# Optimization experiments

Measured on AMD Instinct MI355X. Metric: run time of the kernel, lower is better.

## Reference

```python
import jax, jax.numpy as jnp
import numpy as np

# DeepSeek-style MLA sparse decode: absorbed W_UK/W_UV matmuls in latent space,
# top-k sparse gather from the (kv_lora_rank + rope) latent KV cache.

B, H, S, K = 32, 16, 8192, 2048
L, DN, DR, DV, DM = 512, 128, 64, 128, 2048
SCALE = 1.0 / np.sqrt(DN + DR)  # softmax scale over full qk_head_dim = 192


def setup_inputs() -> dict:
    key = jax.random.key(0)
    ks = jax.random.split(key, 8)
    return {
        "q_nope": jax.random.normal(ks[0], (B, H, DN), dtype=jnp.float32),
        "q_pe": jax.random.normal(ks[1], (B, H, DR), dtype=jnp.float32),  # post-RoPE
        "kv_c": jax.random.normal(ks[2], (B, S, L), dtype=jnp.float32),   # latent cache
        "k_pe": jax.random.normal(ks[3], (B, S, DR), dtype=jnp.float32),  # post-RoPE cache
        "W_UK": jax.random.normal(ks[4], (L, H, DN), dtype=jnp.float32) * 0.02,
        "W_UV": jax.random.normal(ks[5], (L, H, DV), dtype=jnp.float32) * 0.02,
        "W_O": jax.random.normal(ks[6], (H * DV, DM), dtype=jnp.float32) * 0.02,
        "topk_indices": jax.random.randint(ks[7], (B, K), 0, S, dtype=jnp.int32),
    }


def reference(q_nope, q_pe, kv_c, k_pe, W_UK, W_UV, W_O, topk_indices):
    b, h, _ = q_nope.shape
    seq = kv_c.shape[1]
    # absorb q_nope into latent space: [B,H,L]
    q_latent = jnp.einsum('bhd,lhd->bhl', q_nope, W_UK)
    # top-k sparse gather from paged latent cache (-1 == invalid slot)
    valid = topk_indices >= 0                         # [B,K]
    idx = jnp.clip(topk_indices, 0, seq - 1)
    kv_sel = jnp.take_along_axis(kv_c, idx[:, :, None], axis=1)   # [B,K,L]
    kpe_sel = jnp.take_along_axis(k_pe, idx[:, :, None], axis=1)  # [B,K,DR]
    # attention scores: latent part + rope part, fused scale
    scores = (jnp.einsum('bhl,bkl->bhk', q_latent, kv_sel)
              + jnp.einsum('bhr,bkr->bhk', q_pe, kpe_sel)) * SCALE
    scores = jnp.where(valid[:, None, :], scores, -jnp.inf)
    attn = jax.nn.softmax(scores, axis=-1)            # [B,H,K]
    # weighted sum in latent space, then up-project with W_UV
    o_latent = jnp.einsum('bhk,bkl->bhl', attn, kv_sel)
    o = jnp.einsum('bhl,lhv->bhv', o_latent, W_UV)    # [B,H,DV]
    return o.reshape(b, h * o.shape[-1]) @ W_O        # [B,DM]
```

## Files before the change

### kernel.cpp

```cpp
#include <hip/hip_runtime.h>
#include <hip/hip_bf16.h>
#include <cstdint>
#include <cstddef>

constexpr int NB = 32;
constexpr int NH = 16;
constexpr int NS = 8192;
constexpr int NK = 2048;
constexpr int NL = 512;
constexpr int NDR = 64;
constexpr int NDV = 128;
constexpr int NDM = 2048;
constexpr int NDN = 128;
constexpr float SCALE = 0.07216878364870322f;

constexpr int NSPLIT = 32;
constexpr int KC = NK / NSPLIT;
constexpr int ND = NL + NDR;
constexpr int NSUB_D = ND / 16;
constexpr int NS2 = 64;

typedef __attribute__((ext_vector_type(8))) short sh8;
typedef __attribute__((ext_vector_type(4))) float f32x4;

__device__ __forceinline__ short bf16c(float f) {
  union { float f; uint32_t u; } v; v.f = f;
  uint32_t r = v.u + 0x7fffu + ((v.u >> 16) & 1u);
  return (short)(r >> 16);
}

__device__ __forceinline__ float bf2f(short s) {
  union { uint32_t u; float f; } v; v.u = ((uint32_t)(uint16_t)s) << 16;
  return v.f;
}

__device__ __forceinline__ sh8 pack_bf8(float4 a, float4 b) {
  sh8 f;
  f[0] = bf16c(a.x); f[1] = bf16c(a.y); f[2] = bf16c(a.z); f[3] = bf16c(a.w);
  f[4] = bf16c(b.x); f[5] = bf16c(b.y); f[6] = bf16c(b.z); f[7] = bf16c(b.w);
  return f;
}

__global__ __launch_bounds__(256)
void k_qprep(const float* __restrict__ qn,
             const float* __restrict__ qpe,
             const float* __restrict__ wuk,
             short* __restrict__ qle) {
  const int h  = blockIdx.x & 15;
  const int lc = blockIdx.x >> 4;
  const int l0 = lc * 32;
  const int t  = threadIdx.x;
  __shared__ float wlds[32 * 136];
  __shared__ float qlds[32 * 136];

  #pragma unroll
  for (int j = 0; j < 4; ++j) {
    int idx = t + j * 256;
    int li  = idx >> 5;
    int d4  = (idx & 31) * 4;
    *(float4*)&wlds[li * 136 + d4] =
        *(const float4*)&wuk[((size_t)(l0 + li) * NH + h) * NDN + d4];
    *(float4*)&qlds[li * 136 + d4] =
        *(const float4*)&qn[((size_t)li * NH + h) * NDN + d4];
  }
  __syncthreads();

  const int b = t >> 3;
  #pragma unroll
  for (int j = 0; j < 4; ++j) {
    int li = (t & 7) + j * 8;
    float acc = 0.f;
    #pragma unroll
    for (int d4 = 0; d4 < NDN; d4 += 4) {
      float4 wv = *(float4*)&wlds[li * 136 + d4];
      float4 qv = *(float4*)&qlds[b * 136 + d4];
      acc += wv.x * qv.x + wv.y * qv.y + wv.z * qv.z + wv.w * qv.w;
    }
    qle[((size_t)b * NH + h) * ND + l0 + li] = bf16c(acc);
  }
  if (lc == 0) {
    #pragma unroll
    for (int j = 0; j < 8; ++j) {
      int i = t + j * 256;
      int bb = i >> 6, dr = i & 63;
      qle[((size_t)bb * NH + h) * ND + NL + dr] =
          bf16c(qpe[((size_t)bb * NH + h) * NDR + dr]);
    }
  }
}

__global__ __launch_bounds__(256, 2)
void k_attn(const float* __restrict__ kvc,
            const float* __restrict__ kpe,
            const int*   __restrict__ topk,
            const short* __restrict__ qle,
            float* __restrict__ pm,
            float* __restrict__ psum,
            unsigned short* __restrict__ po) {
  const int sp = blockIdx.x;
  const int b  = blockIdx.y;
  const int t  = threadIdx.x;
  const int w  = t >> 6;
  const int lane = t & 63;
  const int lg = lane >> 4;
  const int ln = lane & 15;

  __shared__ __align__(16) short kvs[(KC / 4) * NSUB_D * 64];
  __shared__ __align__(16) short plds[NH * 72];
  __shared__ float mlds[4 * NH];
  __shared__ float slds[4 * NH];

  {
    const int r = t >> 2, c8 = t & 3;
    int idx = topk[(size_t)b * NK + sp * KC + r];
    int id = idx < 0 ? 0 : (idx >= NS ? NS - 1 : idx);
    const float* rowc = kvc + ((size_t)b * NS + id) * NL;
    const float* rowp = kpe + ((size_t)b * NS + id) * NDR;
    #pragma unroll
    for (int g = 0; g < 3; ++g) {
      float4 va[6], vb[6];
      #pragma unroll
      for (int i = 0; i < 6; ++i) {
        int d0 = c8 * 8 + (g * 6 + i) * 32;
        const float* src = (d0 < NL) ? (rowc + d0) : (rowp + (d0 - NL));
        va[i] = *(const float4*)src;
        vb[i] = *(const float4*)(src + 4);
      }
      #pragma unroll
      for (int i = 0; i < 6; ++i) {
        int d0 = c8 * 8 + (g * 6 + i) * 32;
        int s = (r >> 2) * NSUB_D + (d0 >> 4);
        *(sh8*)&kvs[s * 64 + (r & 3) * 16 + (d0 & 15)] = pack_bf8(va[i], vb[i]);
      }
    }
  }
  __syncthreads();

  f32x4 accs = {0.f, 0.f, 0.f, 0.f};
  {
    const short* qrow = qle + ((size_t)b * NH + ln) * ND;
    int k = w * 16 + ln;
    int kbase = (k >> 2) * NSUB_D * 64 + (k & 3) * 16;
    #pragma unroll
    for (int kk = 0; kk < 18; ++kk) {
      int d0 = kk * 32 + lg * 8;
      sh8 qv = *(const sh8*)&qrow[d0];
      sh8 bfr = *(const sh8*)&kvs[kbase + (d0 >> 4) * 64 + (d0 & 15)];
      accs = __builtin_amdgcn_mfma_f32_16x16x32_bf16(qv, bfr, accs, 0, 0, 0);
    }
  }

  const int kq = w * 16 + ln;
  bool valid = topk[(size_t)b * NK + sp * KC + kq] >= 0;
  float sv[4], mx[4];
  #pragma unroll
  for (int q = 0; q < 4; ++q) {
    sv[q] = valid ? accs[q] * SCALE : -INFINITY;
    mx[q] = sv[q];
  }
  #pragma unroll
  for (int off = 1; off < 16; off <<= 1)
    #pragma unroll
    for (int q = 0; q < 4; ++q) mx[q] = fmaxf(mx[q], __shfl_xor(mx[q], off));
  if (ln == 0) {
    #pragma unroll
    for (int q = 0; q < 4; ++q) mlds[w * NH + lg * 4 + q] = mx[q];
  }
  __syncthreads();

  float pr[4], sm[4];
  #pragma unroll
  for (int q = 0; q < 4; ++q) {
    int h = lg * 4 + q;
    float m = fmaxf(fmaxf(mlds[h], mlds[NH + h]),
                    fmaxf(mlds[2 * NH + h], mlds[3 * NH + h]));
    m = fmaxf(m, -1e30f);
    pr[q] = __expf(sv[q] - m);
    sm[q] = pr[q];
  }
  #pragma unroll
  for (int off = 1; off < 16; off <<= 1)
    #pragma unroll
    for (int q = 0; q < 4; ++q) sm[q] += __shfl_xor(sm[q], off);
  if (ln == 0) {
    #pragma unroll
    for (int q = 0; q < 4; ++q) slds[w * NH + lg * 4 + q] = sm[q];
  }
  #pragma unroll
  for (int q = 0; q < 4; ++q)
    plds[(lg * 4 + q) * 72 + kq] = bf16c(pr[q]);
  __syncthreads();

  if (t < NH) {
    float m = fmaxf(fmaxf(mlds[t], mlds[NH + t]),
                    fmaxf(mlds[2 * NH + t], mlds[3 * NH + t]));
    m = fmaxf(m, -1e30f);
    float s = slds[t] + slds[NH + t] + slds[2 * NH + t] + slds[3 * NH + t];
    pm[((size_t)b * NSPLIT + sp) * NH + t] = m;
    psum[((size_t)b * NSPLIT + sp) * NH + t] = s;
  }

  f32x4 acco[8];
  #pragma unroll
  for (int nt = 0; nt < 8; ++nt) acco[nt] = {0.f, 0.f, 0.f, 0.f};

  #pragma unroll
  for (int ks = 0; ks < 2; ++ks) {
    sh8 pa = *(const sh8*)&plds[ln * 72 + ks * 32 + lg * 8];
    int kb = ks * 32 + lg * 8;
    #pragma unroll
    for (int nt = 0; nt < 8; ++nt) {
      int l0 = w * 128 + nt * 16;
      int s = (kb >> 2) * NSUB_D + (l0 >> 4);
      const short* base = &kvs[s * 64 + ln];
      sh8 bv;
      #pragma unroll
      for (int j = 0; j < 4; ++j) bv[j] = base[j * 16];
      #pragma unroll
      for (int j = 0; j < 4; ++j) bv[4 + j] = base[NSUB_D * 64 + j * 16];
      acco[nt] = __builtin_amdgcn_mfma_f32_16x16x32_bf16(pa, bv, acco[nt], 0, 0, 0);
    }
  }

  unsigned short* dst = po + (((size_t)b * NSPLIT + sp) * NH) * NL;
  #pragma unroll
  for (int nt = 0; nt < 8; ++nt) {
    int l = w * 128 + nt * 16 + ln;
    #pragma unroll
    for (int q = 0; q < 4; ++q)
      dst[(size_t)(lg * 4 + q) * NL + l] = (unsigned short)bf16c(acco[nt][q]);
  }
}

__global__ __launch_bounds__(256)
void k_coef(const float* __restrict__ pm,
            const float* __restrict__ psum,
            float* __restrict__ coef) {
  int b = blockIdx.x;
  __shared__ float mm[NSPLIT * NH];
  __shared__ float ssum[NSPLIT * NH];
  int t = threadIdx.x;
  for (int i = t; i < NSPLIT * NH; i += 256) {
    mm[i] = pm[(size_t)b * NSPLIT * NH + i];
    ssum[i] = psum[(size_t)b * NSPLIT * NH + i];
  }
  __syncthreads();
  if (t < NH) {
    float M = -1e30f;
    #pragma unroll
    for (int sp = 0; sp < NSPLIT; ++sp) M = fmaxf(M, mm[sp * NH + t]);
    float S = 0.f;
    #pragma unroll
    for (int sp = 0; sp < NSPLIT; ++sp) S += ssum[sp * NH + t] * __expf(mm[sp * NH + t] - M);
    S = fmaxf(S, 1e-30f);
    #pragma unroll
    for (int sp = 0; sp < NSPLIT; ++sp)
      coef[((size_t)b * NSPLIT + sp) * NH + t] = __expf(mm[sp * NH + t] - M) / S;
  }
}

__global__ __launch_bounds__(256)
void k_combine(const float* __restrict__ coef,
               const unsigned short* __restrict__ po,
               const float* __restrict__ wuv,
               float* __restrict__ ov) {
  int bh = blockIdx.x;
  int b = bh >> 4, h = bh & 15;
  __shared__ float clds[NSPLIT];
  __shared__ float ol[NL];
  __shared__ float red[2][NDV];
  int t = threadIdx.x;
  if (t < NSPLIT) clds[t] = coef[((size_t)b * NSPLIT + t) * NH + h];
  __syncthreads();
  {
    float a0 = 0.f, a1 = 0.f;
    #pragma unroll
    for (int i = 0; i < NSPLIT; ++i) {
      uint32_t pv = *(const uint32_t*)&po[(((size_t)b * NSPLIT + i) * NH + h) * NL + 2 * t];
      a0 += clds[i] * bf2f((short)(pv & 0xffff));
      a1 += clds[i] * bf2f((short)(pv >> 16));
    }
    ol[2 * t] = a0;
    ol[2 * t + 1] = a1;
  }
  __syncthreads();
  {
    int v = t & (NDV - 1);
    int half = t >> 7;
    float a = 0.f;
    #pragma unroll 16
    for (int l = half * 256; l < half * 256 + 256; ++l)
      a += ol[l] * wuv[((size_t)l * NH + h) * NDV + v];
    red[half][v] = a;
  }
  __syncthreads();
  if (t < NDV) ov[(size_t)bh * NDV + t] = red[0][t] + red[1][t];
}

__global__ __launch_bounds__(256)
void k_gemm_part(const float* __restrict__ ov,
                 const float* __restrict__ wo,
                 float* __restrict__ gp) {
  int mc = blockIdx.x;
  int ns = blockIdx.y;
  __shared__ float oc[NB * 32];
  int t = threadIdx.x;
  for (int i = t; i < NB * 32; i += 256) {
    int b = i >> 5, n = i & 31;
    oc[i] = ov[(size_t)b * NDM + ns * 32 + n];
  }
  __syncthreads();
  float acc[NB];
  #pragma unroll
  for (int b = 0; b < NB; ++b) acc[b] = 0.f;
  int m = mc * 256 + t;
  #pragma unroll 8
  for (int n = 0; n < 32; ++n) {
    float wv = wo[(size_t)(ns * 32 + n) * NDM + m];
    #pragma unroll
    for (int b = 0; b < NB; ++b) acc[b] += oc[b * 32 + n] * wv;
  }
  #pragma unroll
  for (int b = 0; b < NB; ++b)
    gp[((size_t)ns * NB + b) * NDM + m] = acc[b];
}

__global__ __launch_bounds__(256)
void k_reduce(const float* __restrict__ gp, float* __restrict__ out) {
  int g = blockIdx.x * 256 + threadIdx.x;
  float a = 0.f;
  #pragma unroll 8
  for (int i = 0; i < NS2; ++i)
    a += gp[(size_t)i * (NB * NDM) + g];
  out[g] = a;
}

extern "C" void kernel_launch(void* const* d_in, const int* in_sizes, int n_in,
                              void* d_out, int out_size, void* d_ws, size_t ws_size,
                              hipStream_t stream) {
  const float* q_nope = (const float*)d_in[0];
  const float* q_pe   = (const float*)d_in[1];
  const float* kv_c   = (const float*)d_in[2];
  const float* k_pe   = (const float*)d_in[3];
  const float* W_UK   = (const float*)d_in[4];
  const float* W_UV   = (const float*)d_in[5];
  const float* W_O    = (const float*)d_in[6];
  const int*   topk   = (const int*)d_in[7];
  float* out = (float*)d_out;

  float* ws = (float*)d_ws;
  short* qle = (short*)ws;
  float* pm   = ws + 147456;
  float* psum = pm + 16384;
  unsigned short* po = (unsigned short*)(psum + 16384);
  float* coef = psum + 16384 + 4194304;
  float* ov   = coef + 16384;
  float* gp   = ov + 65536;

  k_qprep<<<256, 256, 0, stream>>>(q_nope, q_pe, W_UK, qle);
  k_attn<<<dim3(NSPLIT, NB), 256, 0, stream>>>(kv_c, k_pe, topk, qle,
                                               pm, psum, po);
  k_coef<<<NB, 256, 0, stream>>>(pm, psum, coef);
  k_combine<<<NB * NH, 256, 0, stream>>>(coef, po, W_UV, ov);
  k_gemm_part<<<dim3(8, NS2), 256, 0, stream>>>(ov, W_O, gp);
  k_reduce<<<(NB * NDM) / 256, 256, 0, stream>>>(gp, out);
}
```

Before: 90.57 us.

## Fold softmax coefficient kernel into combine and replace split-K reduce with atomics

Removes the separate k_coef kernel by computing the per-split softmax merge coefficients inside k_combine with wavefront shuffles. It also drops the partial-sum buffer and k_reduce kernel, having the W_O GEMM blocks atomically add into a pre-zeroed output instead. This cuts two launches and the 64-way partial-sum write/read traffic (16 MB), at the cost of a memset and 64-way atomic contention per output element plus nondeterministic float summation order.

```diff
diff --git a/kernel.cpp b/kernel.cpp
--- a/kernel.cpp
+++ b/kernel.cpp
@@ -233,34 +233,8 @@
 }
 
 __global__ __launch_bounds__(256)
-void k_coef(const float* __restrict__ pm,
-            const float* __restrict__ psum,
-            float* __restrict__ coef) {
-  int b = blockIdx.x;
-  __shared__ float mm[NSPLIT * NH];
-  __shared__ float ssum[NSPLIT * NH];
-  int t = threadIdx.x;
-  for (int i = t; i < NSPLIT * NH; i += 256) {
-    mm[i] = pm[(size_t)b * NSPLIT * NH + i];
-    ssum[i] = psum[(size_t)b * NSPLIT * NH + i];
-  }
-  __syncthreads();
-  if (t < NH) {
-    float M = -1e30f;
-    #pragma unroll
-    for (int sp = 0; sp < NSPLIT; ++sp) M = fmaxf(M, mm[sp * NH + t]);
-    float S = 0.f;
-    #pragma unroll
-    for (int sp = 0; sp < NSPLIT; ++sp) S += ssum[sp * NH + t] * __expf(mm[sp * NH + t] - M);
-    S = fmaxf(S, 1e-30f);
-    #pragma unroll
-    for (int sp = 0; sp < NSPLIT; ++sp)
-      coef[((size_t)b * NSPLIT + sp) * NH + t] = __expf(mm[sp * NH + t] - M) / S;
-  }
-}
-
-__global__ __launch_bounds__(256)
-void k_combine(const float* __restrict__ coef,
+void k_combine(const float* __restrict__ pm,
+               const float* __restrict__ psum,
                const unsigned short* __restrict__ po,
                const float* __restrict__ wuv,
                float* __restrict__ ov) {
@@ -270,7 +244,17 @@
   __shared__ float ol[NL];
   __shared__ float red[2][NDV];
   int t = threadIdx.x;
-  if (t < NSPLIT) clds[t] = coef[((size_t)b * NSPLIT + t) * NH + h];
+  if (t < NSPLIT) {
+    float m = pm[((size_t)b * NSPLIT + t) * NH + h];
+    float M = m;
+    #pragma unroll
+    for (int off = 16; off; off >>= 1) M = fmaxf(M, __shfl_xor(M, off, 32));
+    float term = psum[((size_t)b * NSPLIT + t) * NH + h] * __expf(m - M);
+    float S = term;
+    #pragma unroll
+    for (int off = 16; off; off >>= 1) S += __shfl_xor(S, off, 32);
+    clds[t] = __expf(m - M) / fmaxf(S, 1e-30f);
+  }
   __syncthreads();
   {
     float a0 = 0.f, a1 = 0.f;
@@ -298,9 +282,9 @@
 }
 
 __global__ __launch_bounds__(256)
-void k_gemm_part(const float* __restrict__ ov,
-                 const float* __restrict__ wo,
-                 float* __restrict__ gp) {
+void k_gemm_atomic(const float* __restrict__ ov,
+                   const float* __restrict__ wo,
+                   float* __restrict__ out) {
   int mc = blockIdx.x;
   int ns = blockIdx.y;
   __shared__ float oc[NB * 32];
@@ -322,17 +306,7 @@
   }
   #pragma unroll
   for (int b = 0; b < NB; ++b)
-    gp[((size_t)ns * NB + b) * NDM + m] = acc[b];
-}
-
-__global__ __launch_bounds__(256)
-void k_reduce(const float* __restrict__ gp, float* __restrict__ out) {
-  int g = blockIdx.x * 256 + threadIdx.x;
-  float a = 0.f;
-  #pragma unroll 8
-  for (int i = 0; i < NS2; ++i)
-    a += gp[(size_t)i * (NB * NDM) + g];
-  out[g] = a;
+    atomicAdd(&out[(size_t)b * NDM + m], acc[b]);
 }
 
 extern "C" void kernel_launch(void* const* d_in, const int* in_sizes, int n_in,
@@ -353,15 +327,12 @@
   float* pm   = ws + 147456;
   float* psum = pm + 16384;
   unsigned short* po = (unsigned short*)(psum + 16384);
-  float* coef = psum + 16384 + 4194304;
-  float* ov   = coef + 16384;
-  float* gp   = ov + 65536;
-
+  float* ov   = psum + 16384 + 4194304;
+
+  hipMemsetAsync(d_out, 0, (size_t)out_size * sizeof(float), stream);
   k_qprep<<<256, 256, 0, stream>>>(q_nope, q_pe, W_UK, qle);
   k_attn<<<dim3(NSPLIT, NB), 256, 0, stream>>>(kv_c, k_pe, topk, qle,
                                                pm, psum, po);
-  k_coef<<<NB, 256, 0, stream>>>(pm, psum, coef);
-  k_combine<<<NB * NH, 256, 0, stream>>>(coef, po, W_UV, ov);
-  k_gemm_part<<<dim3(8, NS2), 256, 0, stream>>>(ov, W_O, gp);
-  k_reduce<<<(NB * NDM) / 256, 256, 0, stream>>>(gp, out);
-}
+  k_combine<<<NB * NH, 256, 0, stream>>>(pm, psum, po, W_UV, ov);
+  k_gemm_atomic<<<dim3(8, NS2), 256, 0, stream>>>(ov, W_O, out);
+}
```

Result: slower. 94.08 us (+3.9%).
